# Kernel optimization log

Measured on AMD Instinct MI355X. Metric: run time of the kernel, lower is better.

Reference implementation:

```python
import jax, jax.numpy as jnp
import numpy as np

IMG = 840.0
MIN_SIZES = [[16.0, 32.0], [64.0, 128.0], [256.0, 512.0]]
STEPS = [8, 16, 32]
THRESH = 0.35      # neg_overlap / matching threshold used by this repo's MultiBoxLoss
NEG_POS = 7
LOC_WEIGHT = 2.0
VAR0, VAR1 = 0.1, 0.2


def _make_priors():
    out = []
    for ms, step in zip(MIN_SIZES, STEPS):
        f = int(np.ceil(IMG / step))
        jj, ii = np.meshgrid(np.arange(f), np.arange(f))  # j: cols (x), i: rows (y)
        cx = (jj + 0.5) * step / IMG
        cy = (ii + 0.5) * step / IMG
        for m in ms:
            s = np.full_like(cx, m / IMG)
            out.append(np.stack([cx, cy, s, s], axis=-1).reshape(-1, 4))
    return np.concatenate(out, axis=0).astype(np.float32)  # [29126, 4] (cx, cy, w, h)


def setup_inputs() -> dict:
    key = jax.random.key(0)
    k1, k2, k3, k4 = jax.random.split(key, 4)
    B, G = 64, 24
    priors = jnp.asarray(_make_priors())            # [P, 4]
    P = priors.shape[0]
    loc_data = 0.1 * jax.random.normal(k1, (B, P, 4), dtype=jnp.float32)
    conf_data = jax.random.normal(k2, (B, P, 2), dtype=jnp.float32)
    cxy = jax.random.uniform(k3, (B, G, 2), minval=0.2, maxval=0.8)
    wh = jax.random.uniform(k4, (B, G, 2), minval=0.05, maxval=0.3)
    gt_boxes = jnp.clip(jnp.concatenate([cxy - wh / 2, cxy + wh / 2], axis=-1), 1e-3, 1.0)
    gt_labels = jnp.ones((B, G), dtype=jnp.int32)   # single foreground class (num_classes=2)
    return {"loc_data": loc_data, "conf_data": conf_data, "gt_boxes": gt_boxes,
            "gt_labels": gt_labels, "priors": priors}


def _multibox_loss(loc_data, conf_data, gt_boxes, gt_labels, priors):
    B, P, _ = loc_data.shape
    G = gt_boxes.shape[1]
    # priors in point form for IoU
    pr_pt = jnp.concatenate([priors[:, :2] - priors[:, 2:] / 2,
                             priors[:, :2] + priors[:, 2:] / 2], axis=1)  # [P,4]
    area_p = (pr_pt[:, 2] - pr_pt[:, 0]) * (pr_pt[:, 3] - pr_pt[:, 1])

    def match_one(truths, labels):
        # IoU [G, P]
        lt = jnp.maximum(truths[:, None, :2], pr_pt[None, :, :2])
        rb = jnp.minimum(truths[:, None, 2:], pr_pt[None, :, 2:])
        wh = jnp.clip(rb - lt, 0.0)
        inter = wh[..., 0] * wh[..., 1]
        area_t = (truths[:, 2] - truths[:, 0]) * (truths[:, 3] - truths[:, 1])
        iou = inter / (area_t[:, None] + area_p[None, :] - inter)
        best_prior_idx = jnp.argmax(iou, axis=1)          # [G]
        bto = jnp.max(iou, axis=0)                        # [P] best truth overlap
        bti = jnp.argmax(iou, axis=0)                     # [P] best truth idx
        bto = bto.at[best_prior_idx].set(2.0)             # ensure each gt keeps its best prior
        bti = bti.at[best_prior_idx].set(jnp.arange(G))
        matched = truths[bti]                             # [P,4]
        conf = jnp.where(bto < THRESH, 0, labels[bti])    # [P]
        # encode (SSD style, variances 0.1/0.2)
        g_cxcy = ((matched[:, :2] + matched[:, 2:]) / 2 - priors[:, :2]) / (VAR0 * priors[:, 2:])
        g_wh = jnp.log((matched[:, 2:] - matched[:, :2]) / priors[:, 2:]) / VAR1
        return jnp.concatenate([g_cxcy, g_wh], axis=1), conf

    loc_t, conf_t = jax.vmap(match_one)(gt_boxes, gt_labels)  # [B,P,4], [B,P]
    pos = conf_t > 0                                          # [B,P]

    # localization: smooth L1 over positives
    diff = jnp.abs(loc_data - loc_t)
    sl1 = jnp.where(diff < 1.0, 0.5 * diff * diff, diff - 0.5)
    loss_l = jnp.sum(sl1 * pos[..., None].astype(loc_data.dtype))

    # per-prior CE = logsumexp - logit[target]
    lse = jax.nn.logsumexp(conf_data, axis=-1)                               # [B,P]
    gold = jnp.take_along_axis(conf_data, conf_t[..., None], axis=-1)[..., 0]
    ce_all = lse - gold                                                      # [B,P]

    # hard negative mining: rank background-class loss of negatives
    mine = jnp.where(pos, 0.0, ce_all)
    rank = jnp.argsort(jnp.argsort(-mine, axis=1), axis=1)
    num_pos = jnp.sum(pos, axis=1, keepdims=True)                            # [B,1]
    num_neg = jnp.minimum(NEG_POS * num_pos, P - 1)
    neg = rank < num_neg

    mask = pos | neg
    loss_c = jnp.sum(jnp.where(mask, ce_all, 0.0))

    N = jnp.maximum(jnp.sum(pos).astype(loc_data.dtype), 1.0)
    return loss_l / N, loss_c / N


def reference(loc_data, conf_data, gt_boxes, gt_labels, priors):
    loss_l, loss_c = _multibox_loss(loc_data, conf_data, gt_boxes, gt_labels, priors)
    return LOC_WEIGHT * loss_l + loss_c
```

## Files before the change

kernel.cpp:

```cpp
#include <hip/hip_runtime.h>

static constexpr int B_ = 64;
static constexpr int P_ = 29126;
static constexpr int G_ = 24;
static constexpr float THRESH_ = 0.35f;
static constexpr int NEGPOS_ = 7;
static constexpr int PBL_ = (P_ + 1023) / 1024;
static constexpr int NBL_ = PBL_ * B_;
static constexpr int CCSTRIDE_ = 32;

__device__ const float LAD_[16] = {
    0.5f,    0.5901f, 0.6964f, 0.8220f, 0.9701f, 1.1450f, 1.3514f, 1.5950f,
    1.8825f, 2.2218f, 2.6223f, 3.0950f, 3.6529f, 4.3113f, 5.0885f, 6.0057f };

static constexpr size_t ZBYTES_ = (size_t)B_*P_ + (size_t)B_*CCSTRIDE_*4;
static constexpr int ZVEC_ = (int)((ZBYTES_ + 15) / 16);

__global__ __launch_bounds__(256) void k_zero(ulonglong2* __restrict__ dst)
{
    const int i = blockIdx.x*256 + threadIdx.x;
    if (i < ZVEC_) dst[i] = make_ulonglong2(0ull, 0ull);
}

__global__ __launch_bounds__(256) void k_sparse(
    const float4* __restrict__ gt4,
    const float4* __restrict__ priors4,
    unsigned char* __restrict__ match,
    unsigned long long* __restrict__ bp_pack)
{
    const int g = blockIdx.x;
    const int b = blockIdx.y;
    const int bg = b*G_ + g;
    const int tid = threadIdx.x;

    const float4 t = gt4[bg];
    const float area_t = (t.z - t.x) * (t.w - t.y);

    float bv = -1.0f; int bq = 0;

#pragma unroll
    for (int r = 0; r < 6; ++r) {
        const int   f    = (r < 2) ? 105 : (r < 4) ? 53 : 27;
        const float sc   = (r < 2) ? 105.0f : (r < 4) ? 52.5f : 26.25f;
        const int   base = (r == 0) ? 0 : (r == 1) ? 11025 : (r == 2) ? 22050
                         : (r == 3) ? 24859 : (r == 4) ? 27668 : 28397;
        const float hw   = ((r == 0) ? 16.0f : (r == 1) ? 32.0f : (r == 2) ? 64.0f
                         : (r == 3) ? 128.0f : (r == 4) ? 256.0f : 512.0f)
                           * (0.5f / 840.0f);

        const int j0 = max(0,     (int)floorf((t.x - hw)*sc - 0.5f) - 1);
        const int j1 = min(f - 1, (int)ceilf ((t.z + hw)*sc - 0.5f) + 1);
        const int i0 = max(0,     (int)floorf((t.y - hw)*sc - 0.5f) - 1);
        const int i1 = min(f - 1, (int)ceilf ((t.w + hw)*sc - 0.5f) + 1);
        const int W = j1 - j0 + 1;
        const int n = W * (i1 - i0 + 1);

        for (int c = tid; c < n; c += 256) {
            const int ii = c / W;
            const int jj = c - ii*W;
            const int p = base + (i0 + ii)*f + (j0 + jj);
            const float4 pr = priors4[p];
            const float hx = pr.z * 0.5f, hy = pr.w * 0.5f;
            const float px0 = pr.x - hx, py0 = pr.y - hy;
            const float px1 = pr.x + hx, py1 = pr.y + hy;
            const float area_p = (px1 - px0) * (py1 - py0);
            const float lx = fmaxf(t.x, px0), ly = fmaxf(t.y, py0);
            const float rx = fminf(t.z, px1), ry = fminf(t.w, py1);
            const float iw = fmaxf(rx - lx, 0.0f), ih = fmaxf(ry - ly, 0.0f);
            const float inter = iw * ih;
            const float iou = __fdividef(inter, (area_t + area_p) - inter);

            if (iou >= THRESH_) match[(size_t)b*P_ + p] = 1;
            if (iou > bv) { bv = iou; bq = p; }
        }
    }

    const int lane = tid & 63, wave = tid >> 6;
    for (int m = 32; m; m >>= 1) {
        const float ov = __shfl_xor(bv, m, 64);
        const int   oq = __shfl_xor(bq, m, 64);
        if (ov > bv || (ov == bv && oq < bq)) { bv = ov; bq = oq; }
    }
    __shared__ float swv[4];
    __shared__ int   swq[4];
    if (lane == 0) { swv[wave] = bv; swq[wave] = bq; }
    __syncthreads();
    if (tid == 0) {
        float v = swv[0]; int q = swq[0];
#pragma unroll
        for (int w = 1; w < 4; ++w)
            if (swv[w] > v || (swv[w] == v && swq[w] < q)) { v = swv[w]; q = swq[w]; }
        bp_pack[bg] = (v >= 0.0f)
            ? (((unsigned long long)__float_as_uint(v) << 32)
               | (unsigned long long)(~(unsigned int)q))
            : 0ull;
    }
}

__global__ __launch_bounds__(256) void k_loss(
    const float4* __restrict__ loc4,
    const float2* __restrict__ conf2,
    const float4* __restrict__ gt4,
    const int* __restrict__ labels,
    const float4* __restrict__ priors4,
    const unsigned char* __restrict__ match,
    const unsigned long long* __restrict__ bp_pack,
    float* __restrict__ mine,
    float* __restrict__ pl, float* __restrict__ pc, int* __restrict__ pp,
    unsigned int* __restrict__ pcnt)
{
    const int b = blockIdx.y;
    const int tid = threadIdx.x;
    const int pbase = blockIdx.x*1024;

    __shared__ float4 sgt[G_];
    __shared__ float  sarea[G_];
    __shared__ int    slab[G_];
    __shared__ signed char sovr[1024];
    if (tid < G_) {
        const float4 t = gt4[b*G_ + tid];
        sgt[tid] = t;
        sarea[tid] = (t.z - t.x) * (t.w - t.y);
        slab[tid] = labels[b*G_ + tid];
    }
    for (int i = tid; i < 1024; i += 256) sovr[i] = -1;
    __syncthreads();
    if (tid == 0) {
        for (int g = 0; g < G_; ++g) {
            const int q = (int)(~(unsigned int)(bp_pack[b*G_ + g] & 0xFFFFFFFFull))
                        - pbase;
            if (q >= 0 && q < 1024) sovr[q] = (signed char)g;
        }
    }
    __syncthreads();

    float lL = 0.0f, pce = 0.0f; int np = 0;
    unsigned q0 = 0, q1 = 0, q2 = 0, q3 = 0, q4 = 0, q5 = 0, q6 = 0, q7 = 0;

#pragma unroll
    for (int c = 0; c < 4; ++c) {
        const int p = pbase + c*256 + tid;
        if (p < P_) {
            const int idx = b*P_ + p;
            const int og = (int)sovr[c*256 + tid];

            int cc = 0, g = 0;
            if (og >= 0) { g = og; cc = slab[g]; }
            else if (match[idx]) {
                const float4 pr = priors4[p];
                const float hx = pr.z * 0.5f, hy = pr.w * 0.5f;
                const float px0 = pr.x - hx, py0 = pr.y - hy;
                const float px1 = pr.x + hx, py1 = pr.y + hy;
                const float area_p = (px1 - px0) * (py1 - py0);
                float best = -1.0f;
#pragma unroll
                for (int gg = 0; gg < G_; ++gg) {
                    const float4 t = sgt[gg];
                    const float lx = fmaxf(t.x, px0), ly = fmaxf(t.y, py0);
                    const float rx = fminf(t.z, px1), ry = fminf(t.w, py1);
                    const float iw = fmaxf(rx - lx, 0.0f), ih = fmaxf(ry - ly, 0.0f);
                    const float inter = iw * ih;
                    const float iou = __fdividef(inter, (sarea[gg] + area_p) - inter);
                    if (iou > best) { best = iou; g = gg; }
                }
                cc = slab[g];
            }

            const float2 x = conf2[idx];
            const float z = (cc == 0) ? (x.y - x.x) : (x.x - x.y);
            const float ce = __logf(1.0f + __expf(z));

            float mv = ce;
            if (cc > 0) {
                np += 1; pce += ce; mv = 0.0f;
                const float4 t  = sgt[g];
                const float4 pr = priors4[p];
                const float gcx = __fdividef((t.x + t.z)*0.5f - pr.x, 0.1f*pr.z);
                const float gcy = __fdividef((t.y + t.w)*0.5f - pr.y, 0.1f*pr.w);
                const float gw  = __logf(__fdividef(t.z - t.x, pr.z)) * 5.0f;
                const float gh  = __logf(__fdividef(t.w - t.y, pr.w)) * 5.0f;
                const float4 l = loc4[idx];
                const float d0 = fabsf(l.x - gcx);
                const float d1 = fabsf(l.y - gcy);
                const float d2 = fabsf(l.z - gw);
                const float d3 = fabsf(l.w - gh);
                lL += (d0 < 1.0f) ? 0.5f*d0*d0 : d0 - 0.5f;
                lL += (d1 < 1.0f) ? 0.5f*d1*d1 : d1 - 0.5f;
                lL += (d2 < 1.0f) ? 0.5f*d2*d2 : d2 - 0.5f;
                lL += (d3 < 1.0f) ? 0.5f*d3*d3 : d3 - 0.5f;
            }
            mine[idx] = mv;

            q0 += (unsigned)(mv > 0.5f)    + ((unsigned)(mv > 0.5901f) << 16);
            q1 += (unsigned)(mv > 0.6964f) + ((unsigned)(mv > 0.8220f) << 16);
            q2 += (unsigned)(mv > 0.9701f) + ((unsigned)(mv > 1.1450f) << 16);
            q3 += (unsigned)(mv > 1.3514f) + ((unsigned)(mv > 1.5950f) << 16);
            q4 += (unsigned)(mv > 1.8825f) + ((unsigned)(mv > 2.2218f) << 16);
            q5 += (unsigned)(mv > 2.6223f) + ((unsigned)(mv > 3.0950f) << 16);
            q6 += (unsigned)(mv > 3.6529f) + ((unsigned)(mv > 4.3113f) << 16);
            q7 += (unsigned)(mv > 5.0885f) + ((unsigned)(mv > 6.0057f) << 16);
        }
    }

    __shared__ float sL[256], sC[256];
    __shared__ int   sP[256];
    __shared__ unsigned su[8][256];
    sL[tid] = lL; sC[tid] = pce; sP[tid] = np;
    su[0][tid] = q0; su[1][tid] = q1; su[2][tid] = q2; su[3][tid] = q3;
    su[4][tid] = q4; su[5][tid] = q5; su[6][tid] = q6; su[7][tid] = q7;
    __syncthreads();
    for (int off = 128; off > 0; off >>= 1) {
        if (tid < off) {
            sL[tid] += sL[tid+off];
            sC[tid] += sC[tid+off];
            sP[tid] += sP[tid+off];
#pragma unroll
            for (int j = 0; j < 8; ++j) su[j][tid] += su[j][tid+off];
        }
        __syncthreads();
    }
    const int o = b*PBL_ + blockIdx.x;
    if (tid == 0) { pl[o] = sL[0]; pc[o] = sC[0]; pp[o] = sP[0]; }
    if (tid < 8) pcnt[o*8 + tid] = su[tid][0];
}

__global__ __launch_bounds__(256) void k_sel1(
    const unsigned int* __restrict__ pcnt, const int* __restrict__ pp,
    int4* __restrict__ sel)
{
    const int b = blockIdx.x;
    const int tid = threadIdx.x;
    __shared__ int sred[256];
    sred[tid] = (tid < PBL_) ? pp[b*PBL_ + tid] : 0;
    __syncthreads();
    for (int off = 128; off > 0; off >>= 1) {
        if (tid < off) sred[tid] += sred[tid+off];
        __syncthreads();
    }
    const int np = sred[0];
    int k = NEGPOS_ * np; if (k > P_-1) k = P_-1;

    __shared__ unsigned red[32][8];
    {
        const int i = tid >> 3, j = tid & 7;
        red[i][j] = (i < PBL_) ? pcnt[(b*PBL_ + i)*8 + j] : 0u;
    }
    __syncthreads();
    for (int off = 16; off > 0; off >>= 1) {
        const int i = tid >> 3, j = tid & 7;
        if (i < off) red[i][j] += red[i+off][j];
        __syncthreads();
    }
    __shared__ int C[16];
    if (tid < 8) {
        C[2*tid]   = (int)(red[0][tid] & 0xFFFFu);
        C[2*tid+1] = (int)(red[0][tid] >> 16);
    }
    __syncthreads();
    if (tid == 0) {
        int4 s; s.w = 0;
        if (k <= 0) {
            s.x = 0x7F800000; s.y = 0x7F800000; s.z = 0;
        } else {
            int js = -1;
            for (int j = 0; j < 16; ++j) if (C[j] >= k) js = j;
            if (js < 0) {
                s.x = __float_as_int(LAD_[0]);
                s.y = __float_as_int(-1.0f);
                s.z = k - C[0];
            } else if (js == 15) {
                s.x = 0x7F800000;
                s.y = __float_as_int(LAD_[15]);
                s.z = k;
            } else {
                s.x = __float_as_int(LAD_[js+1]);
                s.y = __float_as_int(LAD_[js]);
                s.z = k - C[js+1];
            }
        }
        sel[b] = s;
    }
}

__global__ __launch_bounds__(256) void k_collect(
    const float* __restrict__ mine, const int4* __restrict__ sel,
    unsigned int* __restrict__ cand, int* __restrict__ candCount,
    float* __restrict__ pcol)
{
    const int b = blockIdx.y;
    const int tid = threadIdx.x;
    const int lane = tid & 63;
    const int4 se = sel[b];
    const float hi = __int_as_float(se.x);
    const float lo = __int_as_float(se.y);

    __shared__ unsigned int sbuf[1024];
    __shared__ int scnt;
    __shared__ int gbase;
    if (tid == 0) scnt = 0;
    __syncthreads();

    float sum = 0.0f;
#pragma unroll
    for (int c = 0; c < 4; ++c) {
        const int p = blockIdx.x*1024 + c*256 + tid;
        bool isCand = false;
        unsigned int u = 0;
        if (p < P_) {
            const float v = mine[(size_t)b*P_ + p];
            u = __float_as_uint(v);
            if (v > hi) sum += v;
            else isCand = (v > lo);
        }
        const unsigned long long mask = __ballot(isCand);
        const int wcnt = __popcll(mask);
        int wbase = 0;
        if (lane == 0 && wcnt) wbase = atomicAdd(&scnt, wcnt);
        wbase = __shfl(wbase, 0, 64);
        if (isCand) {
            const int before = __popcll(mask & ((1ull << lane) - 1ull));
            sbuf[wbase + before] = u;
        }
    }
    __syncthreads();
    const int tot = scnt;
    if (tid == 0) gbase = tot ? atomicAdd(&candCount[b*CCSTRIDE_], tot) : 0;
    __syncthreads();
    for (int i = tid; i < tot; i += 256)
        cand[(size_t)b*P_ + gbase + i] = sbuf[i];

    __shared__ float sf[256];
    sf[tid] = sum;
    __syncthreads();
    for (int off = 128; off > 0; off >>= 1) {
        if (tid < off) sf[tid] += sf[tid+off];
        __syncthreads();
    }
    if (tid == 0) pcol[b*PBL_ + blockIdx.x] = sf[0];
}

__global__ __launch_bounds__(256) void k_sel2(
    const unsigned int* __restrict__ cand, const int* __restrict__ candCount,
    const int4* __restrict__ sel, const float* __restrict__ pcol,
    float* __restrict__ ctop)
{
    const int b = blockIdx.x;
    const int tid = threadIdx.x;
    __shared__ float sf[256];
    sf[tid] = (tid < PBL_) ? pcol[b*PBL_ + tid] : 0.0f;
    __syncthreads();
    for (int off = 128; off > 0; off >>= 1) {
        if (tid < off) sf[tid] += sf[tid+off];
        __syncthreads();
    }
    const float sumhi = sf[0];
    __syncthreads();

    const int kk = sel[b].z;
    const int nc = candCount[b*CCSTRIDE_];
    if (kk <= 0 || nc <= 0) { if (tid == 0) ctop[b] = sumhi; return; }
    const unsigned int* row = cand + (size_t)b * P_;

    __shared__ unsigned int hist[256];
    __shared__ unsigned int sc0[256], sc1[256];
    __shared__ unsigned int sh_prefix;
    __shared__ int sh_kk;

    unsigned int prefix = 0; int kk2 = kk;
    for (int pass = 3; pass >= 0; --pass) {
        hist[tid] = 0;
        __syncthreads();
        const unsigned int highmask =
            (pass == 3) ? 0u : (0xFFFFFFFFu << ((pass+1)*8));
        for (int i = tid; i < nc; i += 256) {
            const unsigned int u = row[i];
            if ((u & highmask) == (prefix & highmask))
                atomicAdd(&hist[(u >> (pass*8)) & 255u], 1u);
        }
        __syncthreads();
        sc0[tid] = hist[255 - tid];
        __syncthreads();
        unsigned int* src = sc0; unsigned int* dst = sc1;
        for (int off = 1; off < 256; off <<= 1) {
            unsigned int v = src[tid];
            if (tid >= off) v += src[tid - off];
            dst[tid] = v;
            __syncthreads();
            unsigned int* t = src; src = dst; dst = t;
        }
        {
            const int bin = 255 - tid;
            const int cum = (int)src[tid];
            const int cumPrev = (tid == 0) ? 0 : (int)src[tid-1];
            if (cum >= kk2 && cumPrev < kk2) {
                sh_prefix = prefix | ((unsigned int)bin << (pass*8));
                sh_kk = kk2 - cumPrev;
            }
        }
        __syncthreads();
        prefix = sh_prefix; kk2 = sh_kk;
        __syncthreads();
    }

    const float T = __uint_as_float(prefix);
    float sum = 0.0f; int cnt = 0;
    for (int i = tid; i < nc; i += 256) {
        const unsigned int u = row[i];
        if (u > prefix) { sum += __uint_as_float(u); ++cnt; }
    }
    __shared__ int sci[256];
    sf[tid] = sum; sci[tid] = cnt;
    __syncthreads();
    for (int off = 128; off > 0; off >>= 1) {
        if (tid < off) { sf[tid] += sf[tid+off]; sci[tid] += sci[tid+off]; }
        __syncthreads();
    }
    if (tid == 0)
        ctop[b] = sumhi + sf[0] + (float)(kk - sci[0]) * T;
}

__global__ __launch_bounds__(256) void k_final(
    const float* __restrict__ pl, const float* __restrict__ pc,
    const int* __restrict__ pp, const float* __restrict__ ctop,
    float* __restrict__ out)
{
    const int tid = threadIdx.x;
    float sL = 0.0f, sC = 0.0f; int tp = 0;
    for (int i = tid; i < NBL_; i += 256) {
        sL += pl[i]; sC += pc[i]; tp += pp[i];
    }
    float sT = (tid < B_) ? ctop[tid] : 0.0f;
    __shared__ float aL[256], aC[256], aT[256];
    __shared__ int   aP[256];
    aL[tid] = sL; aC[tid] = sC; aT[tid] = sT; aP[tid] = tp;
    __syncthreads();
    for (int off = 128; off > 0; off >>= 1) {
        if (tid < off) {
            aL[tid] += aL[tid+off];
            aC[tid] += aC[tid+off];
            aT[tid] += aT[tid+off];
            aP[tid] += aP[tid+off];
        }
        __syncthreads();
    }
    if (tid == 0) {
        const float N = fmaxf((float)aP[0], 1.0f);
        out[0] = (2.0f*aL[0] + aC[0] + aT[0]) / N;
    }
}

extern "C" void kernel_launch(void* const* d_in, const int* in_sizes, int n_in,
                              void* d_out, int out_size, void* d_ws, size_t ws_size,
                              hipStream_t stream)
{
    const float* loc    = (const float*)d_in[0];
    const float* conf   = (const float*)d_in[1];
    const float* gt     = (const float*)d_in[2];
    const int*   labels = (const int*)d_in[3];
    const float* priors = (const float*)d_in[4];
    float* out = (float*)d_out;

    char* ws = (char*)d_ws;
    size_t off = 0;
    unsigned char* match = (unsigned char*)(ws + off); off += (size_t)B_*P_;
    int* candCount = (int*)(ws + off);                 off += (size_t)B_*CCSTRIDE_*4;
    off = (off + 255) & ~255ull;
    unsigned long long* bp_pack =
        (unsigned long long*)(ws + off);             off += (size_t)B_*G_*8;
    float* mine = (float*)(ws + off);                off += (size_t)B_*P_*4;
    float* pl   = (float*)(ws + off);                off += (size_t)NBL_*4;
    float* pc   = (float*)(ws + off);                off += (size_t)NBL_*4;
    int*   pp   = (int*)(ws + off);                  off += (size_t)NBL_*4;
    float* pcol = (float*)(ws + off);                off += (size_t)NBL_*4;
    unsigned int* pcnt = (unsigned int*)(ws + off);  off += (size_t)NBL_*8*4;
    unsigned int* cand = (unsigned int*)(ws + off);  off += (size_t)B_*P_*4;
    int4*  sel  = (int4*)(ws + off);                 off += (size_t)B_*16;
    float* ctop = (float*)(ws + off);                off += (size_t)B_*4;

    k_zero<<<dim3((ZVEC_ + 255)/256), dim3(256), 0, stream>>>((ulonglong2*)ws);
    k_sparse<<<dim3(G_, B_), dim3(256), 0, stream>>>(
        (const float4*)gt, (const float4*)priors, match, bp_pack);
    k_loss<<<dim3(PBL_, B_), dim3(256), 0, stream>>>(
        (const float4*)loc, (const float2*)conf, (const float4*)gt, labels,
        (const float4*)priors, match, bp_pack, mine, pl, pc, pp, pcnt);
    k_sel1<<<dim3(B_), dim3(256), 0, stream>>>(pcnt, pp, sel);
    k_collect<<<dim3(PBL_, B_), dim3(256), 0, stream>>>(mine, sel, cand, candCount, pcol);
    k_sel2<<<dim3(B_), dim3(256), 0, stream>>>(cand, candCount, sel, pcol, ctop);
    k_final<<<dim3(1), dim3(256), 0, stream>>>(pl, pc, pp, ctop, out);
}
```

Measured before the change: 75.69 us.

## Fuse selection and final reduction kernels, dropping two launches

The per-batch bracket selection (formerly k_sel1) is now recomputed redundantly inside each k_collect block and inside the second-selection kernel. The final global reduction is folded into the second-selection kernel through a last-block ticket pattern. This cuts the pipeline from seven launches to five, removing launch gaps and the single-block final kernel. In exchange every collect block does a small extra reduction over the per-block counts, and a zeroed atomic ticket counter is added to the workspace.

```diff
diff --git a/kernel.cpp b/kernel.cpp
--- a/kernel.cpp
+++ b/kernel.cpp
@@ -13,7 +13,8 @@
     0.5f,    0.5901f, 0.6964f, 0.8220f, 0.9701f, 1.1450f, 1.3514f, 1.5950f,
     1.8825f, 2.2218f, 2.6223f, 3.0950f, 3.6529f, 4.3113f, 5.0885f, 6.0057f };
 
-static constexpr size_t ZBYTES_ = (size_t)B_*P_ + (size_t)B_*CCSTRIDE_*4;
+static constexpr size_t ZBYTES_ =
+    (size_t)B_*P_ + (size_t)B_*CCSTRIDE_*4 + 16;
 static constexpr int ZVEC_ = (int)((ZBYTES_ + 15) / 16);
 
 __global__ __launch_bounds__(256) void k_zero(ulonglong2* __restrict__ dst)
@@ -224,12 +225,10 @@
     if (tid < 8) pcnt[o*8 + tid] = su[tid][0];
 }
 
-__global__ __launch_bounds__(256) void k_sel1(
+__device__ inline void bracket_block(
     const unsigned int* __restrict__ pcnt, const int* __restrict__ pp,
-    int4* __restrict__ sel)
-{
-    const int b = blockIdx.x;
-    const int tid = threadIdx.x;
+    int b, int tid, int4* out, int* np_out)
+{
     __shared__ int sred[256];
     sred[tid] = (tid < PBL_) ? pp[b*PBL_ + tid] : 0;
     __syncthreads();
@@ -256,6 +255,7 @@
         C[2*tid]   = (int)(red[0][tid] & 0xFFFFu);
         C[2*tid+1] = (int)(red[0][tid] >> 16);
     }
+    __shared__ int4 sbr;
     __syncthreads();
     if (tid == 0) {
         int4 s; s.w = 0;
@@ -278,19 +278,25 @@
                 s.z = k - C[js+1];
             }
         }
-        sel[b] = s;
-    }
+        sbr = s;
+    }
+    __syncthreads();
+    *out = sbr;
+    *np_out = np;
 }
 
 __global__ __launch_bounds__(256) void k_collect(
-    const float* __restrict__ mine, const int4* __restrict__ sel,
+    const float* __restrict__ mine,
+    const unsigned int* __restrict__ pcnt, const int* __restrict__ pp,
     unsigned int* __restrict__ cand, int* __restrict__ candCount,
     float* __restrict__ pcol)
 {
     const int b = blockIdx.y;
     const int tid = threadIdx.x;
     const int lane = tid & 63;
-    const int4 se = sel[b];
+
+    int4 se; int np_dummy;
+    bracket_block(pcnt, pp, b, tid, &se, &np_dummy);
     const float hi = __int_as_float(se.x);
     const float lo = __int_as_float(se.y);
 
@@ -329,123 +335,131 @@
     for (int i = tid; i < tot; i += 256)
         cand[(size_t)b*P_ + gbase + i] = sbuf[i];
 
-    __shared__ float sf[256];
-    sf[tid] = sum;
+    __shared__ float sf2[256];
+    sf2[tid] = sum;
     __syncthreads();
     for (int off = 128; off > 0; off >>= 1) {
-        if (tid < off) sf[tid] += sf[tid+off];
+        if (tid < off) sf2[tid] += sf2[tid+off];
         __syncthreads();
     }
-    if (tid == 0) pcol[b*PBL_ + blockIdx.x] = sf[0];
-}
-
-__global__ __launch_bounds__(256) void k_sel2(
+    if (tid == 0) pcol[b*PBL_ + blockIdx.x] = sf2[0];
+}
+
+__global__ __launch_bounds__(256) void k_sel2fin(
     const unsigned int* __restrict__ cand, const int* __restrict__ candCount,
-    const int4* __restrict__ sel, const float* __restrict__ pcol,
-    float* __restrict__ ctop)
+    const unsigned int* __restrict__ pcnt, const int* __restrict__ pp,
+    const float* __restrict__ pl, const float* __restrict__ pc,
+    const float* __restrict__ pcol,
+    float4* __restrict__ outb, unsigned int* __restrict__ ticket,
+    float* __restrict__ out)
 {
     const int b = blockIdx.x;
     const int tid = threadIdx.x;
-    __shared__ float sf[256];
-    sf[tid] = (tid < PBL_) ? pcol[b*PBL_ + tid] : 0.0f;
+
+    int4 se; int np;
+    bracket_block(pcnt, pp, b, tid, &se, &np);
+    const int kk = se.z;
+
+    __shared__ float rA[256], rB[256], rC2[256];
+    rA[tid]  = (tid < PBL_) ? pl[b*PBL_ + tid] : 0.0f;
+    rB[tid]  = (tid < PBL_) ? pc[b*PBL_ + tid] : 0.0f;
+    rC2[tid] = (tid < PBL_) ? pcol[b*PBL_ + tid] : 0.0f;
     __syncthreads();
     for (int off = 128; off > 0; off >>= 1) {
-        if (tid < off) sf[tid] += sf[tid+off];
+        if (tid < off) {
+            rA[tid] += rA[tid+off];
+            rB[tid] += rB[tid+off];
+            rC2[tid] += rC2[tid+off];
+        }
         __syncthreads();
     }
-    const float sumhi = sf[0];
-    __syncthreads();
-
-    const int kk = sel[b].z;
+    const float sumL = rA[0], sumC = rB[0], sumhi = rC2[0];
+    __syncthreads();
+
+    float ctopv = sumhi;
     const int nc = candCount[b*CCSTRIDE_];
-    if (kk <= 0 || nc <= 0) { if (tid == 0) ctop[b] = sumhi; return; }
-    const unsigned int* row = cand + (size_t)b * P_;
-
-    __shared__ unsigned int hist[256];
-    __shared__ unsigned int sc0[256], sc1[256];
-    __shared__ unsigned int sh_prefix;
-    __shared__ int sh_kk;
-
-    unsigned int prefix = 0; int kk2 = kk;
-    for (int pass = 3; pass >= 0; --pass) {
-        hist[tid] = 0;
-        __syncthreads();
-        const unsigned int highmask =
-            (pass == 3) ? 0u : (0xFFFFFFFFu << ((pass+1)*8));
+    if (kk > 0 && nc > 0) {
+        const unsigned int* row = cand + (size_t)b * P_;
+        __shared__ unsigned int hist[256];
+        __shared__ unsigned int sc0[256], sc1[256];
+        __shared__ unsigned int sh_prefix;
+        __shared__ int sh_kk;
+
+        unsigned int prefix = 0; int kk2 = kk;
+        for (int pass = 3; pass >= 0; --pass) {
+            hist[tid] = 0;
+            __syncthreads();
+            const unsigned int highmask =
+                (pass == 3) ? 0u : (0xFFFFFFFFu << ((pass+1)*8));
+            for (int i = tid; i < nc; i += 256) {
+                const unsigned int u = row[i];
+                if ((u & highmask) == (prefix & highmask))
+                    atomicAdd(&hist[(u >> (pass*8)) & 255u], 1u);
+            }
+            __syncthreads();
+            sc0[tid] = hist[255 - tid];
+            __syncthreads();
+            unsigned int* src = sc0; unsigned int* dst = sc1;
+            for (int off = 1; off < 256; off <<= 1) {
+                unsigned int v = src[tid];
+                if (tid >= off) v += src[tid - off];
+                dst[tid] = v;
+                __syncthreads();
+                unsigned int* t2 = src; src = dst; dst = t2;
+            }
+            {
+                const int bin = 255 - tid;
+                const int cum = (int)src[tid];
+                const int cumPrev = (tid == 0) ? 0 : (int)src[tid-1];
+                if (cum >= kk2 && cumPrev < kk2) {
+                    sh_prefix = prefix | ((unsigned int)bin << (pass*8));
+                    sh_kk = kk2 - cumPrev;
+                }
+            }
+            __syncthreads();
+            prefix = sh_prefix; kk2 = sh_kk;
+            __syncthreads();
+        }
+
+        const float T = __uint_as_float(prefix);
+        float sum = 0.0f; int cnt = 0;
         for (int i = tid; i < nc; i += 256) {
             const unsigned int u = row[i];
-            if ((u & highmask) == (prefix & highmask))
-                atomicAdd(&hist[(u >> (pass*8)) & 255u], 1u);
-        }
+            if (u > prefix) { sum += __uint_as_float(u); ++cnt; }
+        }
+        __shared__ float sf[256];
+        __shared__ int   sci[256];
+        sf[tid] = sum; sci[tid] = cnt;
         __syncthreads();
-        sc0[tid] = hist[255 - tid];
-        __syncthreads();
-        unsigned int* src = sc0; unsigned int* dst = sc1;
-        for (int off = 1; off < 256; off <<= 1) {
-            unsigned int v = src[tid];
-            if (tid >= off) v += src[tid - off];
-            dst[tid] = v;
+        for (int off = 128; off > 0; off >>= 1) {
+            if (tid < off) { sf[tid] += sf[tid+off]; sci[tid] += sci[tid+off]; }
             __syncthreads();
-            unsigned int* t = src; src = dst; dst = t;
-        }
-        {
-            const int bin = 255 - tid;
-            const int cum = (int)src[tid];
-            const int cumPrev = (tid == 0) ? 0 : (int)src[tid-1];
-            if (cum >= kk2 && cumPrev < kk2) {
-                sh_prefix = prefix | ((unsigned int)bin << (pass*8));
-                sh_kk = kk2 - cumPrev;
-            }
-        }
-        __syncthreads();
-        prefix = sh_prefix; kk2 = sh_kk;
-        __syncthreads();
-    }
-
-    const float T = __uint_as_float(prefix);
-    float sum = 0.0f; int cnt = 0;
-    for (int i = tid; i < nc; i += 256) {
-        const unsigned int u = row[i];
-        if (u > prefix) { sum += __uint_as_float(u); ++cnt; }
-    }
-    __shared__ int sci[256];
-    sf[tid] = sum; sci[tid] = cnt;
-    __syncthreads();
-    for (int off = 128; off > 0; off >>= 1) {
-        if (tid < off) { sf[tid] += sf[tid+off]; sci[tid] += sci[tid+off]; }
-        __syncthreads();
-    }
-    if (tid == 0)
-        ctop[b] = sumhi + sf[0] + (float)(kk - sci[0]) * T;
-}
-
-__global__ __launch_bounds__(256) void k_final(
-    const float* __restrict__ pl, const float* __restrict__ pc,
-    const int* __restrict__ pp, const float* __restrict__ ctop,
-    float* __restrict__ out)
-{
-    const int tid = threadIdx.x;
-    float sL = 0.0f, sC = 0.0f; int tp = 0;
-    for (int i = tid; i < NBL_; i += 256) {
-        sL += pl[i]; sC += pc[i]; tp += pp[i];
-    }
-    float sT = (tid < B_) ? ctop[tid] : 0.0f;
-    __shared__ float aL[256], aC[256], aT[256];
-    __shared__ int   aP[256];
-    aL[tid] = sL; aC[tid] = sC; aT[tid] = sT; aP[tid] = tp;
-    __syncthreads();
-    for (int off = 128; off > 0; off >>= 1) {
-        if (tid < off) {
-            aL[tid] += aL[tid+off];
-            aC[tid] += aC[tid+off];
-            aT[tid] += aT[tid+off];
-            aP[tid] += aP[tid+off];
-        }
-        __syncthreads();
-    }
+        }
+        ctopv = sumhi + sf[0] + (float)(kk - sci[0]) * T;
+    }
+
+    __shared__ int sdone;
     if (tid == 0) {
-        const float N = fmaxf((float)aP[0], 1.0f);
-        out[0] = (2.0f*aL[0] + aC[0] + aT[0]) / N;
+        outb[b] = make_float4(sumL, sumC, (float)np, ctopv);
+        __threadfence();
+        sdone = (int)atomicAdd(ticket, 1u);
+    }
+    __syncthreads();
+    if (sdone == B_ - 1) {
+        __threadfence();
+        float L = 0.0f, C = 0.0f, Pn = 0.0f, T = 0.0f;
+        if (tid < B_) {
+            const float4 v = outb[tid];
+            L = v.x; C = v.y; Pn = v.z; T = v.w;
+        }
+        for (int m = 32; m; m >>= 1) {
+            L += __shfl_xor(L, m, 64);
+            C += __shfl_xor(C, m, 64);
+            Pn += __shfl_xor(Pn, m, 64);
+            T += __shfl_xor(T, m, 64);
+        }
+        if (tid == 0)
+            out[0] = (2.0f*L + C + T) / fmaxf(Pn, 1.0f);
     }
 }
 
@@ -464,6 +478,7 @@
     size_t off = 0;
     unsigned char* match = (unsigned char*)(ws + off); off += (size_t)B_*P_;
     int* candCount = (int*)(ws + off);                 off += (size_t)B_*CCSTRIDE_*4;
+    unsigned int* ticket = (unsigned int*)(ws + off);  off += 16;
     off = (off + 255) & ~255ull;
     unsigned long long* bp_pack =
         (unsigned long long*)(ws + off);             off += (size_t)B_*G_*8;
@@ -474,8 +489,7 @@
     float* pcol = (float*)(ws + off);                off += (size_t)NBL_*4;
     unsigned int* pcnt = (unsigned int*)(ws + off);  off += (size_t)NBL_*8*4;
     unsigned int* cand = (unsigned int*)(ws + off);  off += (size_t)B_*P_*4;
-    int4*  sel  = (int4*)(ws + off);                 off += (size_t)B_*16;
-    float* ctop = (float*)(ws + off);                off += (size_t)B_*4;
+    float4* outb = (float4*)(ws + off);              off += (size_t)B_*16;
 
     k_zero<<<dim3((ZVEC_ + 255)/256), dim3(256), 0, stream>>>((ulonglong2*)ws);
     k_sparse<<<dim3(G_, B_), dim3(256), 0, stream>>>(
@@ -483,8 +497,8 @@
     k_loss<<<dim3(PBL_, B_), dim3(256), 0, stream>>>(
         (const float4*)loc, (const float2*)conf, (const float4*)gt, labels,
         (const float4*)priors, match, bp_pack, mine, pl, pc, pp, pcnt);
-    k_sel1<<<dim3(B_), dim3(256), 0, stream>>>(pcnt, pp, sel);
-    k_collect<<<dim3(PBL_, B_), dim3(256), 0, stream>>>(mine, sel, cand, candCount, pcol);
-    k_sel2<<<dim3(B_), dim3(256), 0, stream>>>(cand, candCount, sel, pcol, ctop);
-    k_final<<<dim3(1), dim3(256), 0, stream>>>(pl, pc, pp, ctop, out);
-}
+    k_collect<<<dim3(PBL_, B_), dim3(256), 0, stream>>>(
+        mine, pcnt, pp, cand, candCount, pcol);
+    k_sel2fin<<<dim3(B_), dim3(256), 0, stream>>>(
+        cand, candCount, pcnt, pp, pl, pc, pcol, outb, ticket, out);
+}
```

After: 76.34 us. Within noise of the previous version (+0.9%).
